# Performance work log

Hardware: AMD Instinct MI355X
Metric: run time of the kernel (lower is better)

Reference implementation:

```python
import jax, jax.numpy as jnp
import numpy as np
from jax import lax

NUM_CHANNELS = 32
PROT_SECTION = 4
PROT_SIZE = NUM_CHANNELS * PROT_SECTION  # 128
BATCH = 128
SEQ_LEN = 8194


def setup_inputs() -> dict:
    key = jax.random.key(0)
    ks = jax.random.split(key, 6)
    input_seq = jax.random.randint(ks[0], (BATCH, SEQ_LEN), 0, 26)
    emb = jax.random.normal(ks[1], (26, 5), dtype=jnp.float32)
    conv_w = jax.random.normal(ks[2], (NUM_CHANNELS, 5, 3), dtype=jnp.float32) * 0.1
    conv_b = jnp.zeros((NUM_CHANNELS,), dtype=jnp.float32)
    W_a = jax.random.normal(ks[3], (PROT_SIZE, PROT_SIZE), dtype=jnp.float32) / np.sqrt(PROT_SIZE)
    v_a = jax.random.normal(ks[4], (PROT_SIZE,), dtype=jnp.float32)
    return {"input_seq": input_seq, "emb": emb, "conv_w": conv_w,
            "conv_b": conv_b, "W_a": W_a, "v_a": v_a}


def reference(input_seq, emb, conv_w, conv_b, W_a, v_a):
    # Embedding lookup: [B, L, 5] -> [B, 5, L]
    x = emb[input_seq].transpose(0, 2, 1)
    # Conv1d(5 -> C, k=3, valid) + bias + ReLU  (dropout is identity in eval)
    y = lax.conv_general_dilated(x, conv_w, window_strides=(1,), padding='VALID',
                                 dimension_numbers=('NCH', 'OIH', 'NCH'))
    y = jax.nn.relu(y + conv_b[None, :, None])  # [B, C, L-2]
    B, C, PL = y.shape
    S = PROT_SECTION
    new_L = PL // S
    rem = PL % S
    head = rem // 2
    tail = PL - (rem - head)
    y = y[:, :, head:tail].reshape(B, C * S, new_L)  # [B, D, N], D = C*S
    # Batched self-attention pooling (original loops over batch in Python)
    # energies[b, n] = v_a @ tanh(W_a @ H_b)
    e = jnp.einsum('d,bdn->bn', v_a, jnp.tanh(jnp.einsum('de,ben->bdn', W_a, y)))
    w = jax.nn.softmax(e, axis=-1)  # stable softmax; same math as unstable F.softmax
    ctx = jnp.einsum('bn,bdn->bd', w, y)  # [B, D]
    return ctx
```

## Files before the change

### kernel.cpp

```cpp
#include <hip/hip_runtime.h>

#define LSEQ 8194
#define NPOS 2048

typedef _Float16 f16x8 __attribute__((ext_vector_type(8)));
typedef _Float16 f16x2 __attribute__((ext_vector_type(2)));
typedef __attribute__((ext_vector_type(4))) float f32x4;

static __device__ __forceinline__ float tanh_fast(float x){
    float p = __expf(2.0f * x);
    float r = __builtin_amdgcn_rcpf(1.0f + p);
    return 1.0f - 2.0f * r;
}
static __device__ __forceinline__ unsigned h3relu(unsigned a, unsigned b, unsigned c){
    union { f16x2 h; unsigned u; } x, y, z, r;
    x.u = a; y.u = b; z.u = c;
    f16x2 s = x.h + y.h + z.h;
    f16x2 zero = { (_Float16)0.0f, (_Float16)0.0f };
    r.h = __builtin_elementwise_max(s, zero);
    return r.u;
}
static __device__ __forceinline__ unsigned hpack(float a, float b){
    union { f16x2 h; unsigned u; } pk;
    pk.h = (f16x2){ (_Float16)a, (_Float16)b };
    return pk.u;
}

__global__ __launch_bounds__(256) void k_tbl(
        const float* __restrict__ emb, const float* __restrict__ cw,
        const float* __restrict__ cb, const float* __restrict__ Wa,
        unsigned* __restrict__ tblp, unsigned* __restrict__ wah)
{
    int gid = blockIdx.x*256 + threadIdx.x;
    if (gid < 1248){
        int k = gid / 416;
        int rem = gid - k*416;
        int l = rem >> 4;
        int cp = rem & 15;
        int c0 = cp*2;
        float v0 = 0.f, v1 = 0.f;
        #pragma unroll
        for (int i = 0; i < 5; i++){
            float e = emb[l*5 + i];
            v0 += cw[(c0*5 + i)*3 + k] * e;
            v1 += cw[((c0+1)*5 + i)*3 + k] * e;
        }
        if (k == 2){ v0 += cb[c0]; v1 += cb[c0+1]; }
        tblp[k*520 + l*20 + (cp & 3)*4 + (cp >> 2)] = hpack(v0, v1);
    }
    for (int i = gid; i < 8192; i += 1280)
        wah[i] = hpack(Wa[2*i], Wa[2*i + 1]);
}

__global__ __launch_bounds__(256, 4) void k_fused(
        const int* __restrict__ seq, const unsigned* __restrict__ tblp,
        const unsigned* __restrict__ wah, const float* __restrict__ va,
        float* __restrict__ part, float* __restrict__ stats)
{
    __shared__ __align__(16) unsigned tblH[1560];
    __shared__ unsigned short seqw16[4][260];
    __shared__ uint4 bshare[16*64];
    __shared__ float epar[4][64];
    __shared__ float elds[256];
    __shared__ float wlds[256];
    __shared__ float red[4], red2[4];
    __shared__ float red3[4][4][32];

    int tid = threadIdx.x;
    int b   = blockIdx.y;
    int x   = blockIdx.x;
    int n0  = x * 256;

    for (int i = tid; i < 390; i += 256)
        ((uint4*)tblH)[i] = ((const uint4*)tblp)[i];
    const int* sb = seq + (size_t)b * LSEQ;
    for (int i = tid; i < 4*258; i += 256){
        int s = i / 258, off = i - s*258;
        seqw16[s][off] = (unsigned short)(sb[s*2048 + n0 + off] * 80);
    }

    int w = tid >> 6, lane = tid & 63;
    int m = lane & 15, q = lane >> 4;

    uint4 wfu[2][4];
    #pragma unroll
    for (int dtL = 0; dtL < 2; dtL++)
        #pragma unroll
        for (int ki = 0; ki < 4; ki++)
            wfu[dtL][ki] = *(const uint4*)((const char*)wah +
                ((2*w+dtL)*16 + m)*256 + ki*64 + q*16);
    float varg[2][4];
    #pragma unroll
    for (int dtL = 0; dtL < 2; dtL++)
        #pragma unroll
        for (int r = 0; r < 4; r++)
            varg[dtL][r] = va[(2*w+dtL)*16 + q*4 + r];
    __syncthreads();

    const char* tb0 = (const char*)tblH + q*16;
    const char* tb1 = tb0 + 2080;
    const char* tb2 = tb1 + 2080;

    for (int sub = 0; sub < 4; sub++){
        int row = sub*64 + w*16 + m;
        unsigned o0[4], o1[4], o2[4];
        #pragma unroll
        for (int s = 0; s < 4; s++){
            o0[s] = seqw16[s][row];
            o1[s] = seqw16[s][row+1];
            o2[s] = seqw16[s][row+2];
        }
        unsigned V[4][4];
        #pragma unroll
        for (int s = 0; s < 4; s++){
            uint4 t0 = *(const uint4*)(tb0 + o0[s]);
            uint4 t1 = *(const uint4*)(tb1 + o1[s]);
            uint4 t2 = *(const uint4*)(tb2 + o2[s]);
            V[s][0] = h3relu(t0.x, t1.x, t2.x);
            V[s][1] = h3relu(t0.y, t1.y, t2.y);
            V[s][2] = h3relu(t0.z, t1.z, t2.z);
            V[s][3] = h3relu(t0.w, t1.w, t2.w);
        }
        #pragma unroll
        for (int ki = 0; ki < 4; ki++){
            uint4 o;
            o.x = __builtin_amdgcn_perm(V[1][ki], V[0][ki], 0x05040100u);
            o.y = __builtin_amdgcn_perm(V[3][ki], V[2][ki], 0x05040100u);
            o.z = __builtin_amdgcn_perm(V[1][ki], V[0][ki], 0x07060302u);
            o.w = __builtin_amdgcn_perm(V[3][ki], V[2][ki], 0x07060302u);
            bshare[(w*4 + ki)*64 + lane] = o;
        }
        __syncthreads();

        f32x4 acc[2][4];
        #pragma unroll
        for (int dtL = 0; dtL < 2; dtL++)
            #pragma unroll
            for (int rg = 0; rg < 4; rg++) acc[dtL][rg] = (f32x4){0.f,0.f,0.f,0.f};
        #pragma unroll
        for (int rg = 0; rg < 4; rg++){
            #pragma unroll
            for (int ki = 0; ki < 4; ki++){
                union { uint4 u; f16x8 f; } bu, a0, a1;
                bu.u = bshare[(rg*4 + ki)*64 + lane];
                a0.u = wfu[0][ki];
                a1.u = wfu[1][ki];
                acc[0][rg] = __builtin_amdgcn_mfma_f32_16x16x32_f16(a0.f, bu.f, acc[0][rg], 0, 0, 0);
                acc[1][rg] = __builtin_amdgcn_mfma_f32_16x16x32_f16(a1.f, bu.f, acc[1][rg], 0, 0, 0);
            }
        }
        #pragma unroll
        for (int rg = 0; rg < 4; rg++){
            float ep = 0.f;
            #pragma unroll
            for (int dtL = 0; dtL < 2; dtL++){
                ep += varg[dtL][0] * tanh_fast(acc[dtL][rg][0]);
                ep += varg[dtL][1] * tanh_fast(acc[dtL][rg][1]);
                ep += varg[dtL][2] * tanh_fast(acc[dtL][rg][2]);
                ep += varg[dtL][3] * tanh_fast(acc[dtL][rg][3]);
            }
            ep += __shfl_xor(ep, 16);
            ep += __shfl_xor(ep, 32);
            if (lane < 16) epar[w][rg*16 + lane] = ep;
        }
        __syncthreads();
        if (tid < 64)
            elds[sub*64 + tid] = epar[0][tid] + epar[1][tid] + epar[2][tid] + epar[3][tid];
    }
    __syncthreads();

    float ev = elds[tid];
    float mx = ev;
    #pragma unroll
    for (int off = 32; off >= 1; off >>= 1) mx = fmaxf(mx, __shfl_xor(mx, off));
    if (lane == 0) red[w] = mx;
    __syncthreads();
    mx = fmaxf(fmaxf(red[0], red[1]), fmaxf(red[2], red[3]));
    float wgt_own = __expf(ev - mx);
    float sum = wgt_own;
    #pragma unroll
    for (int off = 32; off >= 1; off >>= 1) sum += __shfl_xor(sum, off);
    if (lane == 0) red2[w] = sum;
    wlds[tid] = wgt_own;
    __syncthreads();
    float s_x = red2[0] + red2[1] + red2[2] + red2[3];

    int qq = tid & 3, nn = tid >> 2;
    const char* t0 = (const char*)tblH + qq*16;
    const char* t1 = t0 + 2080;
    const char* t2 = t1 + 2080;
    float acc[32];
    #pragma unroll
    for (int j = 0; j < 32; j++) acc[j] = 0.f;
    for (int it = 0; it < 4; it++){
        int n = it*64 + nn;
        float wgt = wlds[n];
        unsigned o0[4], o1[4], o2[4];
        #pragma unroll
        for (int s = 0; s < 4; s++){
            o0[s] = seqw16[s][n];
            o1[s] = seqw16[s][n+1];
            o2[s] = seqw16[s][n+2];
        }
        #pragma unroll
        for (int s = 0; s < 4; s++){
            uint4 a = *(const uint4*)(t0 + o0[s]);
            uint4 bb = *(const uint4*)(t1 + o1[s]);
            uint4 c = *(const uint4*)(t2 + o2[s]);
            union { f16x2 h; unsigned u; } u0, u1, u2, u3;
            u0.u = h3relu(a.x, bb.x, c.x);
            u1.u = h3relu(a.y, bb.y, c.y);
            u2.u = h3relu(a.z, bb.z, c.z);
            u3.u = h3relu(a.w, bb.w, c.w);
            acc[0*8 + 0*4 + s] += wgt * (float)u0.h[0];
            acc[0*8 + 1*4 + s] += wgt * (float)u0.h[1];
            acc[1*8 + 0*4 + s] += wgt * (float)u1.h[0];
            acc[1*8 + 1*4 + s] += wgt * (float)u1.h[1];
            acc[2*8 + 0*4 + s] += wgt * (float)u2.h[0];
            acc[2*8 + 1*4 + s] += wgt * (float)u2.h[1];
            acc[3*8 + 0*4 + s] += wgt * (float)u3.h[0];
            acc[3*8 + 1*4 + s] += wgt * (float)u3.h[1];
        }
    }
    #pragma unroll
    for (int j = 0; j < 32; j++){
        acc[j] += __shfl_xor(acc[j], 4);
        acc[j] += __shfl_xor(acc[j], 8);
        acc[j] += __shfl_xor(acc[j], 16);
        acc[j] += __shfl_xor(acc[j], 32);
    }
    if (lane < 4){
        #pragma unroll
        for (int j = 0; j < 32; j++) red3[w][lane][j] = acc[j];
    }
    __syncthreads();
    if (tid < 128){
        int ki = tid >> 5, q2 = (tid >> 3) & 3, par = (tid >> 2) & 1, s = tid & 3;
        int a = ki*8 + par*4 + s;
        part[((size_t)b*8 + x)*128 + tid] =
            red3[0][q2][a] + red3[1][q2][a] + red3[2][q2][a] + red3[3][q2][a];
    }
    if (tid == 0){
        stats[((size_t)b*8 + x)*2    ] = mx;
        stats[((size_t)b*8 + x)*2 + 1] = s_x;
    }
}

__global__ __launch_bounds__(128) void kb2_finish(const float* __restrict__ part,
        const float* __restrict__ stats, float* __restrict__ out)
{
    int b = blockIdx.x, d = threadIdx.x;
    const float* st = stats + (size_t)b*16;
    float M = -1e30f;
    #pragma unroll
    for (int x = 0; x < 8; x++) M = fmaxf(M, st[x*2]);
    float f[8], S = 0.f;
    #pragma unroll
    for (int x = 0; x < 8; x++){
        f[x] = __expf(st[x*2] - M);
        S += st[x*2+1] * f[x];
    }
    float inv = 1.0f / S;
    const float* p = part + (size_t)b*8*128 + d;
    float s = 0.f;
    #pragma unroll
    for (int x = 0; x < 8; x++) s += p[x*128] * f[x];
    out[b*128 + d] = s * inv;
}

extern "C" void kernel_launch(void* const* d_in, const int* in_sizes, int n_in,
                              void* d_out, int out_size, void* d_ws, size_t ws_size,
                              hipStream_t stream)
{
    const int*   seq = (const int*)d_in[0];
    const float* emb = (const float*)d_in[1];
    const float* cw  = (const float*)d_in[2];
    const float* cb  = (const float*)d_in[3];
    const float* Wa  = (const float*)d_in[4];
    const float* va  = (const float*)d_in[5];
    float* out = (float*)d_out;

    char* wsb = (char*)d_ws;
    float*    part  = (float*)wsb;
    float*    stats = (float*)(wsb + (1<<20));
    unsigned* tblp  = (unsigned*)(wsb + (2<<20));
    unsigned* wah   = (unsigned*)(wsb + (2<<20) + 16384);

    k_tbl     <<<5,           256, 0, stream>>>(emb, cw, cb, Wa, tblp, wah);
    k_fused   <<<dim3(8,128), 256, 0, stream>>>(seq, tblp, wah, va, part, stats);
    kb2_finish<<<128,         128, 0, stream>>>(part, stats, out);
}
```

Measured before the change: 98.34 us.

## Fuse weighted context accumulation into the energy loop with online softmax

Replaces the separate post-energy pass, which recomputed conv outputs from the LDS table to build the weighted context, with an online-softmax accumulation inside the sub-tile loop. Each sub-tile reuses its already computed V registers, rescaling the running accumulators by alpha whenever the running max changes. This removes the second round of table gathers and h3relu work plus one block reduction phase. In exchange it adds a per-sub-tile serial max and sum step on the first wave, an extra barrier per iteration, and 32 more live registers during the MFMA loop, which could reduce occupancy.

Result: slower. 102.3 us (+4.0%).

```diff
diff --git a/kernel.cpp b/kernel.cpp
--- a/kernel.cpp
+++ b/kernel.cpp
@@ -61,10 +61,9 @@
     __shared__ unsigned short seqw16[4][260];
     __shared__ uint4 bshare[16*64];
     __shared__ float epar[4][64];
-    __shared__ float elds[256];
-    __shared__ float wlds[256];
-    __shared__ float red[4], red2[4];
+    __shared__ float wsub[64];
     __shared__ float red3[4][4][32];
+    __shared__ float Mlds, Slds, Alds;
 
     int tid = threadIdx.x;
     int b   = blockIdx.y;
@@ -78,6 +77,7 @@
         int s = i / 258, off = i - s*258;
         seqw16[s][off] = (unsigned short)(sb[s*2048 + n0 + off] * 80);
     }
+    if (tid == 0){ Mlds = -3e38f; Slds = 0.f; }
 
     int w = tid >> 6, lane = tid & 63;
     int m = lane & 15, q = lane >> 4;
@@ -100,6 +100,10 @@
     const char* tb0 = (const char*)tblH + q*16;
     const char* tb1 = tb0 + 2080;
     const char* tb2 = tb1 + 2080;
+
+    float accp[32];
+    #pragma unroll
+    for (int j = 0; j < 32; j++) accp[j] = 0.f;
 
     for (int sub = 0; sub < 4; sub++){
         int row = sub*64 + w*16 + m;
@@ -164,74 +168,52 @@
             if (lane < 16) epar[w][rg*16 + lane] = ep;
         }
         __syncthreads();
-        if (tid < 64)
-            elds[sub*64 + tid] = epar[0][tid] + epar[1][tid] + epar[2][tid] + epar[3][tid];
-    }
-    __syncthreads();
-
-    float ev = elds[tid];
-    float mx = ev;
-    #pragma unroll
-    for (int off = 32; off >= 1; off >>= 1) mx = fmaxf(mx, __shfl_xor(mx, off));
-    if (lane == 0) red[w] = mx;
-    __syncthreads();
-    mx = fmaxf(fmaxf(red[0], red[1]), fmaxf(red[2], red[3]));
-    float wgt_own = __expf(ev - mx);
-    float sum = wgt_own;
-    #pragma unroll
-    for (int off = 32; off >= 1; off >>= 1) sum += __shfl_xor(sum, off);
-    if (lane == 0) red2[w] = sum;
-    wlds[tid] = wgt_own;
-    __syncthreads();
-    float s_x = red2[0] + red2[1] + red2[2] + red2[3];
-
-    int qq = tid & 3, nn = tid >> 2;
-    const char* t0 = (const char*)tblH + qq*16;
-    const char* t1 = t0 + 2080;
-    const char* t2 = t1 + 2080;
-    float acc[32];
-    #pragma unroll
-    for (int j = 0; j < 32; j++) acc[j] = 0.f;
-    for (int it = 0; it < 4; it++){
-        int n = it*64 + nn;
-        float wgt = wlds[n];
-        unsigned o0[4], o1[4], o2[4];
+
+        if (tid < 64){
+            float e4 = epar[0][tid] + epar[1][tid] + epar[2][tid] + epar[3][tid];
+            float msub = e4;
+            #pragma unroll
+            for (int off = 32; off >= 1; off >>= 1)
+                msub = fmaxf(msub, __shfl_xor(msub, off));
+            float Mold = Mlds;
+            float Mnew = fmaxf(Mold, msub);
+            float wr = __expf(e4 - Mnew);
+            wsub[tid] = wr;
+            float ssub = wr;
+            #pragma unroll
+            for (int off = 32; off >= 1; off >>= 1) ssub += __shfl_xor(ssub, off);
+            if (tid == 0){
+                float alpha = __expf(Mold - Mnew);
+                Alds = alpha;
+                Slds = alpha * Slds + ssub;
+                Mlds = Mnew;
+            }
+        }
+        __syncthreads();
+
+        float alpha = Alds;
+        float wr = wsub[w*16 + m];
         #pragma unroll
         for (int s = 0; s < 4; s++){
-            o0[s] = seqw16[s][n];
-            o1[s] = seqw16[s][n+1];
-            o2[s] = seqw16[s][n+2];
-        }
-        #pragma unroll
-        for (int s = 0; s < 4; s++){
-            uint4 a = *(const uint4*)(t0 + o0[s]);
-            uint4 bb = *(const uint4*)(t1 + o1[s]);
-            uint4 c = *(const uint4*)(t2 + o2[s]);
-            union { f16x2 h; unsigned u; } u0, u1, u2, u3;
-            u0.u = h3relu(a.x, bb.x, c.x);
-            u1.u = h3relu(a.y, bb.y, c.y);
-            u2.u = h3relu(a.z, bb.z, c.z);
-            u3.u = h3relu(a.w, bb.w, c.w);
-            acc[0*8 + 0*4 + s] += wgt * (float)u0.h[0];
-            acc[0*8 + 1*4 + s] += wgt * (float)u0.h[1];
-            acc[1*8 + 0*4 + s] += wgt * (float)u1.h[0];
-            acc[1*8 + 1*4 + s] += wgt * (float)u1.h[1];
-            acc[2*8 + 0*4 + s] += wgt * (float)u2.h[0];
-            acc[2*8 + 1*4 + s] += wgt * (float)u2.h[1];
-            acc[3*8 + 0*4 + s] += wgt * (float)u3.h[0];
-            acc[3*8 + 1*4 + s] += wgt * (float)u3.h[1];
-        }
-    }
+            #pragma unroll
+            for (int ki = 0; ki < 4; ki++){
+                union { f16x2 h; unsigned u; } uv; uv.u = V[s][ki];
+                accp[ki*8 + s]     = alpha * accp[ki*8 + s]     + wr * (float)uv.h[0];
+                accp[ki*8 + 4 + s] = alpha * accp[ki*8 + 4 + s] + wr * (float)uv.h[1];
+            }
+        }
+    }
+
     #pragma unroll
     for (int j = 0; j < 32; j++){
-        acc[j] += __shfl_xor(acc[j], 4);
-        acc[j] += __shfl_xor(acc[j], 8);
-        acc[j] += __shfl_xor(acc[j], 16);
-        acc[j] += __shfl_xor(acc[j], 32);
-    }
-    if (lane < 4){
-        #pragma unroll
-        for (int j = 0; j < 32; j++) red3[w][lane][j] = acc[j];
+        accp[j] += __shfl_xor(accp[j], 1);
+        accp[j] += __shfl_xor(accp[j], 2);
+        accp[j] += __shfl_xor(accp[j], 4);
+        accp[j] += __shfl_xor(accp[j], 8);
+    }
+    if (m == 0){
+        #pragma unroll
+        for (int j = 0; j < 32; j++) red3[w][q][j] = accp[j];
     }
     __syncthreads();
     if (tid < 128){
@@ -241,8 +223,8 @@
             red3[0][q2][a] + red3[1][q2][a] + red3[2][q2][a] + red3[3][q2][a];
     }
     if (tid == 0){
-        stats[((size_t)b*8 + x)*2    ] = mx;
-        stats[((size_t)b*8 + x)*2 + 1] = s_x;
+        stats[((size_t)b*8 + x)*2    ] = Mlds;
+        stats[((size_t)b*8 + x)*2 + 1] = Slds;
     }
 }
 
```
